# Performance work log

Hardware: AMD Instinct MI355X
Metric: run time of the kernel (lower is better)

The kernel has to match this reference:

```python
import jax, jax.numpy as jnp
import numpy as np

EPS = 1e-5

def _graph_conv(x, src, dst, W, b, N):
    # DGL GraphConv, norm='both': D_out^{-1/2} then aggregate then D_in^{-1/2}
    ones = jnp.ones((src.shape[0],), x.dtype)
    out_deg = jnp.clip(jax.ops.segment_sum(ones, src, num_segments=N), 1.0)
    in_deg = jnp.clip(jax.ops.segment_sum(ones, dst, num_segments=N), 1.0)
    h = (x * (out_deg ** -0.5)[:, None]) @ W          # [N, out] (mult W before gather)
    agg = jax.ops.segment_sum(h[src], dst, num_segments=N)  # [N, out] irregular scatter
    return agg * (in_deg ** -0.5)[:, None] + b

def _bn_relu(h, gamma, beta):
    # BatchNorm1d in training mode: batch stats over node axis (biased var)
    mu = jnp.mean(h, axis=0)
    var = jnp.mean((h - mu) ** 2, axis=0)
    return jax.nn.relu((h - mu) * jax.lax.rsqrt(var + EPS) * gamma + beta)

def setup_inputs() -> dict:
    key = jax.random.key(0)
    ks = jax.random.split(key, 6)
    N, E, F, H, C = 100000, 1000000, 128, 128, 16
    return {
        "x": jax.random.normal(ks[0], (N, F), dtype=jnp.float32),
        "src": jax.random.randint(ks[1], (E,), 0, N, dtype=jnp.int32),
        "dst": jax.random.randint(ks[2], (E,), 0, N, dtype=jnp.int32),
        "W1": jax.random.normal(ks[3], (F, H), dtype=jnp.float32) * 0.05,
        "b1": jnp.zeros((H,), jnp.float32),
        "g1": jnp.ones((H,), jnp.float32),
        "be1": jnp.zeros((H,), jnp.float32),
        "W2": jax.random.normal(ks[4], (H, H), dtype=jnp.float32) * 0.05,
        "b2": jnp.zeros((H,), jnp.float32),
        "g2": jnp.ones((H,), jnp.float32),
        "be2": jnp.zeros((H,), jnp.float32),
        "Wc": jax.random.normal(ks[5], (H, C), dtype=jnp.float32) * 0.05,
        "bc": jnp.zeros((C,), jnp.float32),
    }

def reference(x, src, dst, W1, b1, g1, be1, W2, b2, g2, be2, Wc, bc):
    N = x.shape[0]
    h = _bn_relu(_graph_conv(x, src, dst, W1, b1, N), g1, be1)  # dropout = identity (eval)
    h = _bn_relu(_graph_conv(h, src, dst, W2, b2, N), g2, be2)
    return h @ Wc + bc  # [N, num_cls]
```

## Files before the change

kernel.cpp:

```cpp
#include <hip/hip_runtime.h>

#define FDIM 128
#define MAXDEG 64
#define GATHERB 2048
#define NREP 32

typedef unsigned short ushort_t;
typedef unsigned int uint_t;
typedef __attribute__((ext_vector_type(8))) short short8;
typedef __attribute__((ext_vector_type(16))) float float16;

__device__ __forceinline__ float bflo(uint_t u) { return __uint_as_float(u << 16); }
__device__ __forceinline__ float bfhi(uint_t u) { return __uint_as_float(u & 0xffff0000u); }
__device__ __forceinline__ ushort_t f2bf(float f) {
    uint_t u = __float_as_uint(f);
    return (ushort_t)((u + 0x7fffu + ((u >> 16) & 1u)) >> 16);
}
__device__ __forceinline__ uint_t pack2bf(float lo, float hi) {
    return (uint_t)f2bf(lo) | ((uint_t)f2bf(hi) << 16);
}

__global__ __launch_bounds__(256) void mega1_kernel(
    const float* __restrict__ x, const float* __restrict__ W,
    const int* __restrict__ src, const int* __restrict__ dst,
    int* __restrict__ cs, int* __restrict__ cursor, int* __restrict__ eidx,
    ushort_t* __restrict__ outb, int N, int E,
    int gemmB, int atomicB) {
    int bid = blockIdx.x;
    int t = threadIdx.x;

    int six = atomicB * 6;
    bool isAtomic;
    int idx;
    if (bid < six) {
        int grp = bid / 6, rem = bid % 6;
        if (rem == 5) { isAtomic = true; idx = grp; }
        else { isAtomic = false; idx = grp * 5 + rem; }
    } else {
        isAtomic = false;
        idx = atomicB * 5 + (bid - six);
    }

    if (isAtomic) {
        int stride = atomicB * 256;
        for (int i = idx * 256 + t; i < E; i += stride) {
            int d = dst[i];
            int s = src[i];
            int slot = atomicAdd(&cursor[d], 1);
            if (slot < MAXDEG) eidx[(size_t)d * MAXDEG + slot] = s;
            atomicAdd(&cs[s], 1);
        }
        return;
    }

    if (idx >= gemmB) return;
    __shared__ float xt[16][FDIM];
    int base = idx * 16;
    const float4* x4 = (const float4*)x;
#pragma unroll
    for (int i = 0; i < 2; i++) {
        int ii = t + i * 256;
        int row = ii >> 5, c4 = ii & 31;
        int grow = base + row;
        float4 v = make_float4(0.f, 0.f, 0.f, 0.f);
        if (grow < N) v = x4[(size_t)grow * 32 + c4];
        *(float4*)&xt[row][c4 * 4] = v;
    }
    __syncthreads();
    int rg = t >> 6, c = t & 63;
    float acc[4][2] = {};
    const float* Wc0 = W + c;
    for (int k4 = 0; k4 < 32; k4++) {
        float xv[16];
#pragma unroll
        for (int r = 0; r < 4; r++) {
            float4 tmp = *(const float4*)&xt[rg * 4 + r][k4 * 4];
            xv[r * 4 + 0] = tmp.x; xv[r * 4 + 1] = tmp.y;
            xv[r * 4 + 2] = tmp.z; xv[r * 4 + 3] = tmp.w;
        }
#pragma unroll
        for (int kk = 0; kk < 4; kk++) {
            float w0 = Wc0[(k4 * 4 + kk) * FDIM];
            float w1 = Wc0[(k4 * 4 + kk) * FDIM + 64];
#pragma unroll
            for (int r = 0; r < 4; r++) {
                acc[r][0] = fmaf(xv[r * 4 + kk], w0, acc[r][0]);
                acc[r][1] = fmaf(xv[r * 4 + kk], w1, acc[r][1]);
            }
        }
    }
#pragma unroll
    for (int r = 0; r < 4; r++) {
        int grow = base + rg * 4 + r;
        if (grow < N) {
            outb[(size_t)grow * FDIM + c] = f2bf(acc[r][0]);
            outb[(size_t)grow * FDIM + c + 64] = f2bf(acc[r][1]);
        }
    }
}

template <bool OS>
__global__ __launch_bounds__(256) void gather_kernel(const ushort_t* __restrict__ hb,
                                                     const int* __restrict__ eidx,
                                                     const int* __restrict__ cnt,
                                                     const int* __restrict__ cs,
                                                     const float* __restrict__ b,
                                                     ushort_t* __restrict__ outb,
                                                     float* __restrict__ statsRep, int N) {
    __shared__ float4 redS[256];
    __shared__ float4 redQ[256];
    int t = threadIdx.x;
    int wave = t >> 6, lane = t & 63;
    int half = lane >> 5, sub = lane & 31;
    int gw = blockIdx.x * 4 + wave;
    const uint2* h2 = (const uint2*)hb;
    uint2* o2 = (uint2*)outb;
    float4 bb = ((const float4*)b)[sub];
    float st0 = 0, st1 = 0, st2 = 0, st3 = 0, sq0 = 0, sq1 = 0, sq2 = 0, sq3 = 0;

    for (int node = gw; node < N; node += GATHERB * 4) {
        int deg = cnt[node];
        int e = min(deg, MAXDEG);
        const int* row = eidx + (size_t)node * MAXDEG;
        int ridx = (lane < e) ? row[lane] : 0;
        float scv = 1.f;
        if (OS) scv = (lane < e) ? rsqrtf((float)max(cs[ridx], 1)) : 0.f;

        float a0 = 0, a1 = 0, a2 = 0, a3 = 0;
        float c0 = 0, c1 = 0, c2 = 0, c3 = 0;
        int j = 0;
        for (; j + 3 < e; j += 4) {
            int iA = __shfl(ridx, j + half);
            int iB = __shfl(ridx, j + 2 + half);
            float sA = OS ? __shfl(scv, j + half) : 1.f;
            float sB = OS ? __shfl(scv, j + 2 + half) : 1.f;
            uint2 uA = h2[(size_t)iA * 32 + sub];
            uint2 uB = h2[(size_t)iB * 32 + sub];
            a0 = fmaf(bflo(uA.x), sA, a0); a1 = fmaf(bfhi(uA.x), sA, a1);
            a2 = fmaf(bflo(uA.y), sA, a2); a3 = fmaf(bfhi(uA.y), sA, a3);
            c0 = fmaf(bflo(uB.x), sB, c0); c1 = fmaf(bfhi(uB.x), sB, c1);
            c2 = fmaf(bflo(uB.y), sB, c2); c3 = fmaf(bfhi(uB.y), sB, c3);
        }
        for (; j < e; j += 2) {
            int jj = j + half;
            bool take = jj < e;
            int i0 = __shfl(ridx, take ? jj : (e - 1));
            float s0 = take ? (OS ? __shfl(scv, jj) : 1.f) : 0.f;
            uint2 u = h2[(size_t)i0 * 32 + sub];
            a0 = fmaf(bflo(u.x), s0, a0); a1 = fmaf(bfhi(u.x), s0, a1);
            a2 = fmaf(bflo(u.y), s0, a2); a3 = fmaf(bfhi(u.y), s0, a3);
        }
        a0 += c0; a1 += c1; a2 += c2; a3 += c3;
        a0 += __shfl_xor(a0, 32);
        a1 += __shfl_xor(a1, 32);
        a2 += __shfl_xor(a2, 32);
        a3 += __shfl_xor(a3, 32);
        if (half == 0) {
            float isc = rsqrtf((float)max(deg, 1));
            uint2 o;
            o.x = pack2bf(fmaf(a0, isc, bb.x), fmaf(a1, isc, bb.y));
            o.y = pack2bf(fmaf(a2, isc, bb.z), fmaf(a3, isc, bb.w));
            o2[(size_t)node * 32 + sub] = o;
            float v0 = bflo(o.x), v1 = bfhi(o.x), v2 = bflo(o.y), v3 = bfhi(o.y);
            st0 += v0; st1 += v1; st2 += v2; st3 += v3;
            sq0 = fmaf(v0, v0, sq0); sq1 = fmaf(v1, v1, sq1);
            sq2 = fmaf(v2, v2, sq2); sq3 = fmaf(v3, v3, sq3);
        }
    }

    redS[t] = make_float4(st0, st1, st2, st3);
    redQ[t] = make_float4(sq0, sq1, sq2, sq3);
    __syncthreads();
    if (t < 32) {
        float4 s = make_float4(0, 0, 0, 0), q = make_float4(0, 0, 0, 0);
#pragma unroll
        for (int w = 0; w < 4; w++) {
            float4 a = redS[w * 64 + t];
            float4 z = redQ[w * 64 + t];
            s.x += a.x; s.y += a.y; s.z += a.z; s.w += a.w;
            q.x += z.x; q.y += z.y; q.z += z.z; q.w += z.w;
        }
        float* dstp = statsRep + (size_t)(blockIdx.x & (NREP - 1)) * 256;
        atomicAdd(&dstp[t * 4 + 0], s.x);
        atomicAdd(&dstp[t * 4 + 1], s.y);
        atomicAdd(&dstp[t * 4 + 2], s.z);
        atomicAdd(&dstp[t * 4 + 3], s.w);
        atomicAdd(&dstp[128 + t * 4 + 0], q.x);
        atomicAdd(&dstp[128 + t * 4 + 1], q.y);
        atomicAdd(&dstp[128 + t * 4 + 2], q.z);
        atomicAdd(&dstp[128 + t * 4 + 3], q.w);
    }
}

__global__ __launch_bounds__(256) void gemm2_kernel(const ushort_t* __restrict__ hb,
                                                    const float* __restrict__ W,
                                                    const int* __restrict__ cs,
                                                    const float* __restrict__ statsRep,
                                                    const float* __restrict__ g,
                                                    const float* __restrict__ be,
                                                    ushort_t* __restrict__ outb, int N,
                                                    float invN) {
    __shared__ ushort_t zt[64][136];
    __shared__ ushort_t wt[128][136];
    __shared__ float Ash[FDIM], Bsh[FDIM];
    int t = threadIdx.x;
    int base = blockIdx.x * 64;

    if (t < FDIM) {
        float s = 0.f, q = 0.f;
        for (int r = 0; r < NREP; r++) {
            s += statsRep[r * 256 + t];
            q += statsRep[r * 256 + 128 + t];
        }
        float mu = s * invN;
        float var = q * invN - mu * mu;
        float a = g[t] * rsqrtf(var + 1e-5f);
        Ash[t] = a;
        Bsh[t] = be[t] - mu * a;
    }
    for (int i = t; i < FDIM * FDIM; i += 256) {
        int k = i >> 7, n = i & 127;
        wt[n][k] = f2bf(W[i]);
    }
    __syncthreads();

    const uint_t* h1 = (const uint_t*)hb;
    for (int i = t; i < 64 * 64; i += 256) {
        int row = i >> 6, cp = i & 63;
        int grow = base + row;
        uint_t o = 0;
        if (grow < N) {
            uint_t u = h1[(size_t)grow * 64 + cp];
            float s = rsqrtf((float)max(cs[grow], 1));
            float v0 = fmaxf(fmaf(bflo(u), Ash[cp * 2], Bsh[cp * 2]), 0.f) * s;
            float v1 = fmaxf(fmaf(bfhi(u), Ash[cp * 2 + 1], Bsh[cp * 2 + 1]), 0.f) * s;
            o = pack2bf(v0, v1);
        }
        *(uint_t*)&zt[row][cp * 2] = o;
    }
    __syncthreads();

    int wv = t >> 6, lane = t & 63;
    int rt = wv >> 1;
    int m = lane & 31;
    int kg = lane >> 5;

    short8 af[8];
#pragma unroll
    for (int kk = 0; kk < 8; kk++)
        af[kk] = *(const short8*)&zt[rt * 32 + m][kk * 16 + kg * 8];

#pragma unroll
    for (int cc = 0; cc < 2; cc++) {
        int ct = (wv & 1) * 2 + cc;
        float16 acc = {0, 0, 0, 0, 0, 0, 0, 0, 0, 0, 0, 0, 0, 0, 0, 0};
#pragma unroll
        for (int kk = 0; kk < 8; kk++) {
            short8 bf = *(const short8*)&wt[ct * 32 + m][kk * 16 + kg * 8];
            acc = __builtin_amdgcn_mfma_f32_32x32x16_bf16(af[kk], bf, acc, 0, 0, 0);
        }
        int col = ct * 32 + m;
#pragma unroll
        for (int r = 0; r < 16; r++) {
            int row = base + rt * 32 + (r & 3) + 8 * (r >> 2) + 4 * kg;
            if (row < N) outb[(size_t)row * FDIM + col] = f2bf(acc[r]);
        }
    }
}

__global__ __launch_bounds__(256) void cls_kernel(const ushort_t* __restrict__ hb,
                                                  const float* __restrict__ Wc,
                                                  const float* __restrict__ bc,
                                                  const float* __restrict__ statsRep,
                                                  const float* __restrict__ g,
                                                  const float* __restrict__ be,
                                                  float* __restrict__ out, int N, float invN) {
    __shared__ float wcl[FDIM * 16];
    __shared__ float red[16][256];
    __shared__ float Ash[FDIM], Bsh[FDIM];
    int t = threadIdx.x;
    int base = blockIdx.x * 64;
#pragma unroll
    for (int i = 0; i < 8; i++) wcl[t + i * 256] = Wc[t + i * 256];
    if (t < FDIM) {
        float s = 0.f, q = 0.f;
        for (int r = 0; r < NREP; r++) {
            s += statsRep[r * 256 + t];
            q += statsRep[r * 256 + 128 + t];
        }
        float mu = s * invN;
        float var = q * invN - mu * mu;
        float a = g[t] * rsqrtf(var + 1e-5f);
        Ash[t] = a;
        Bsh[t] = be[t] - mu * a;
    }
    __syncthreads();

    int node = base + (t >> 2);
    int q4 = t & 3;
    float acc[16];
#pragma unroll
    for (int c = 0; c < 16; c++) acc[c] = 0.f;

    if (node < N) {
        const uint2* hu2 = (const uint2*)((const uint_t*)hb + (size_t)node * 64 + q4 * 16);
        const float* Af = Ash + q4 * 32;
        const float* Bf = Bsh + q4 * 32;
#pragma unroll 1
        for (int kk = 0; kk < 8; kk++) {
            uint2 u = hu2[kk];
            float4 ab = *(const float4*)&Af[kk * 4];
            float4 bb = *(const float4*)&Bf[kk * 4];
            float v0 = fmaxf(fmaf(bflo(u.x), ab.x, bb.x), 0.f);
            float v1 = fmaxf(fmaf(bfhi(u.x), ab.y, bb.y), 0.f);
            float v2 = fmaxf(fmaf(bflo(u.y), ab.z, bb.z), 0.f);
            float v3 = fmaxf(fmaf(bfhi(u.y), ab.w, bb.w), 0.f);
            int k0 = q4 * 32 + kk * 4;
            const float* w0 = &wcl[k0 * 16];
#pragma unroll
            for (int c = 0; c < 16; c++) {
                float s = fmaf(v0, w0[c], fmaf(v1, w0[16 + c], fmaf(v2, w0[32 + c], v3 * w0[48 + c])));
                acc[c] += s;
            }
        }
    }
#pragma unroll
    for (int c = 0; c < 16; c++) red[c][t] = acc[c];
    __syncthreads();
#pragma unroll
    for (int i = t; i < 64 * 16; i += 256) {
        int n = i >> 4, c = i & 15;
        float4 p = *(const float4*)&red[c][n * 4];
        int grow = base + n;
        if (grow < N) out[(size_t)grow * 16 + c] = (p.x + p.y) + (p.z + p.w) + bc[c];
    }
}

extern "C" void kernel_launch(void* const* d_in, const int* in_sizes, int n_in,
                              void* d_out, int out_size, void* d_ws, size_t ws_size,
                              hipStream_t stream) {
    const float* x  = (const float*)d_in[0];
    const int* src  = (const int*)d_in[1];
    const int* dst  = (const int*)d_in[2];
    const float* W1 = (const float*)d_in[3];
    const float* b1 = (const float*)d_in[4];
    const float* g1 = (const float*)d_in[5];
    const float* be1= (const float*)d_in[6];
    const float* W2 = (const float*)d_in[7];
    const float* b2 = (const float*)d_in[8];
    const float* g2 = (const float*)d_in[9];
    const float* be2= (const float*)d_in[10];
    const float* Wc = (const float*)d_in[11];
    const float* bc = (const float*)d_in[12];
    float* out = (float*)d_out;

    int N = in_sizes[0] / FDIM;
    int E = in_sizes[1];
    size_t NB = (size_t)N * FDIM;

    ushort_t* bufA = (ushort_t*)d_ws;
    ushort_t* bufB = bufA + NB;
    int* cs        = (int*)(bufB + NB);
    int* cursor    = cs + N;
    float* statsR1 = (float*)(cursor + N);
    float* statsR2 = statsR1 + NREP * 256;
    int* eidx      = (int*)(statsR2 + NREP * 256);

    hipMemsetAsync(cs, 0, ((size_t)2 * N + 2 * NREP * 256) * sizeof(int), stream);

    int gemmB = (N + 15) / 16;
    int atomicB = (gemmB + 4) / 5;
    int totalB = gemmB + atomicB;

    mega1_kernel<<<totalB, 256, 0, stream>>>(
        x, W1, src, dst, cs, cursor, eidx, bufA, N, E, gemmB, atomicB);

    float invN = 1.0f / N;

    gather_kernel<true><<<GATHERB, 256, 0, stream>>>(bufA, eidx, cursor, cs, b1, bufB, statsR1, N);

    gemm2_kernel<<<(N + 63) / 64, 256, 0, stream>>>(bufB, W2, cs, statsR1, g1, be1, bufA, N, invN);
    gather_kernel<false><<<GATHERB, 256, 0, stream>>>(bufA, eidx, cursor, nullptr, b2, bufB, statsR2, N);

    cls_kernel<<<(N + 63) / 64, 256, 0, stream>>>(bufB, Wc, bc, statsR2, g2, be2, out, N, invN);
}
```

Measured before the change: 380.7 us.

## Assign one node per half-wave in gather kernel instead of one per wave

The gather kernel now processes two nodes per wave, one per 32-lane half, instead of splitting one node's edges across both halves. This removes the cross-half shuffle reduction and lets every half-wave write and accumulate statistics, and the block reduction is adjusted to sum 8 groups of 32 lanes. Each half now walks its node's neighbour list serially with 4-way unrolling. Degree imbalance between the two nodes sharing a wave can cause divergence, and nodes with more than 32 edges fall back to a slower scalar loop.

```diff
diff --git a/kernel.cpp b/kernel.cpp
--- a/kernel.cpp
+++ b/kernel.cpp
@@ -112,28 +112,61 @@
     int t = threadIdx.x;
     int wave = t >> 6, lane = t & 63;
     int half = lane >> 5, sub = lane & 31;
-    int gw = blockIdx.x * 4 + wave;
+    int hofs = half * 32;
     const uint2* h2 = (const uint2*)hb;
     uint2* o2 = (uint2*)outb;
     float4 bb = ((const float4*)b)[sub];
     float st0 = 0, st1 = 0, st2 = 0, st3 = 0, sq0 = 0, sq1 = 0, sq2 = 0, sq3 = 0;
 
-    for (int node = gw; node < N; node += GATHERB * 4) {
-        int deg = cnt[node];
+    int pairCount = (N + 1) >> 1;
+    for (int p = blockIdx.x * 4 + wave; p < pairCount; p += GATHERB * 4) {
+        int node = 2 * p + half;
+        bool valid = node < N;
+        int deg = valid ? cnt[node] : 0;
         int e = min(deg, MAXDEG);
-        const int* row = eidx + (size_t)node * MAXDEG;
-        int ridx = (lane < e) ? row[lane] : 0;
-        float scv = 1.f;
-        if (OS) scv = (lane < e) ? rsqrtf((float)max(cs[ridx], 1)) : 0.f;
+        int e1 = min(e, 32);
+
+        const int* rowSelf = eidx + (size_t)node * MAXDEG;
+        int ridx = (valid && sub < e) ? rowSelf[sub] : 0;
+        float scv = 0.f;
+        if (OS) scv = (valid && sub < e) ? rsqrtf((float)max(cs[ridx], 1)) : 0.f;
+        int ridx2 = 0;
+        float scv2 = 0.f;
+        if (e > 32) {
+            ridx2 = (sub + 32 < e) ? rowSelf[32 + sub] : 0;
+            if (OS) scv2 = (sub + 32 < e) ? rsqrtf((float)max(cs[ridx2], 1)) : 0.f;
+        }
 
         float a0 = 0, a1 = 0, a2 = 0, a3 = 0;
         float c0 = 0, c1 = 0, c2 = 0, c3 = 0;
         int j = 0;
-        for (; j + 3 < e; j += 4) {
-            int iA = __shfl(ridx, j + half);
-            int iB = __shfl(ridx, j + 2 + half);
-            float sA = OS ? __shfl(scv, j + half) : 1.f;
-            float sB = OS ? __shfl(scv, j + 2 + half) : 1.f;
+        for (; j + 3 < e1; j += 4) {
+            int iA = __shfl(ridx, hofs + j);
+            int iB = __shfl(ridx, hofs + j + 1);
+            int iC = __shfl(ridx, hofs + j + 2);
+            int iD = __shfl(ridx, hofs + j + 3);
+            float sA = OS ? __shfl(scv, hofs + j) : 1.f;
+            float sB = OS ? __shfl(scv, hofs + j + 1) : 1.f;
+            float sC = OS ? __shfl(scv, hofs + j + 2) : 1.f;
+            float sD = OS ? __shfl(scv, hofs + j + 3) : 1.f;
+            uint2 uA = h2[(size_t)iA * 32 + sub];
+            uint2 uB = h2[(size_t)iB * 32 + sub];
+            uint2 uC = h2[(size_t)iC * 32 + sub];
+            uint2 uD = h2[(size_t)iD * 32 + sub];
+            a0 = fmaf(bflo(uA.x), sA, a0); a1 = fmaf(bfhi(uA.x), sA, a1);
+            a2 = fmaf(bflo(uA.y), sA, a2); a3 = fmaf(bfhi(uA.y), sA, a3);
+            c0 = fmaf(bflo(uB.x), sB, c0); c1 = fmaf(bfhi(uB.x), sB, c1);
+            c2 = fmaf(bflo(uB.y), sB, c2); c3 = fmaf(bfhi(uB.y), sB, c3);
+            a0 = fmaf(bflo(uC.x), sC, a0); a1 = fmaf(bfhi(uC.x), sC, a1);
+            a2 = fmaf(bflo(uC.y), sC, a2); a3 = fmaf(bfhi(uC.y), sC, a3);
+            c0 = fmaf(bflo(uD.x), sD, c0); c1 = fmaf(bfhi(uD.x), sD, c1);
+            c2 = fmaf(bflo(uD.y), sD, c2); c3 = fmaf(bfhi(uD.y), sD, c3);
+        }
+        for (; j + 1 < e1; j += 2) {
+            int iA = __shfl(ridx, hofs + j);
+            int iB = __shfl(ridx, hofs + j + 1);
+            float sA = OS ? __shfl(scv, hofs + j) : 1.f;
+            float sB = OS ? __shfl(scv, hofs + j + 1) : 1.f;
             uint2 uA = h2[(size_t)iA * 32 + sub];
             uint2 uB = h2[(size_t)iB * 32 + sub];
             a0 = fmaf(bflo(uA.x), sA, a0); a1 = fmaf(bfhi(uA.x), sA, a1);
@@ -141,21 +174,24 @@
             c0 = fmaf(bflo(uB.x), sB, c0); c1 = fmaf(bfhi(uB.x), sB, c1);
             c2 = fmaf(bflo(uB.y), sB, c2); c3 = fmaf(bfhi(uB.y), sB, c3);
         }
-        for (; j < e; j += 2) {
-            int jj = j + half;
-            bool take = jj < e;
-            int i0 = __shfl(ridx, take ? jj : (e - 1));
-            float s0 = take ? (OS ? __shfl(scv, jj) : 1.f) : 0.f;
-            uint2 u = h2[(size_t)i0 * 32 + sub];
-            a0 = fmaf(bflo(u.x), s0, a0); a1 = fmaf(bfhi(u.x), s0, a1);
-            a2 = fmaf(bflo(u.y), s0, a2); a3 = fmaf(bfhi(u.y), s0, a3);
+        if (j < e1) {
+            int iA = __shfl(ridx, hofs + j);
+            float sA = OS ? __shfl(scv, hofs + j) : 1.f;
+            uint2 uA = h2[(size_t)iA * 32 + sub];
+            a0 = fmaf(bflo(uA.x), sA, a0); a1 = fmaf(bfhi(uA.x), sA, a1);
+            a2 = fmaf(bflo(uA.y), sA, a2); a3 = fmaf(bfhi(uA.y), sA, a3);
+            j++;
+        }
+        for (j = 32; j < e; j++) {
+            int iA = __shfl(ridx2, hofs + (j - 32));
+            float sA = OS ? __shfl(scv2, hofs + (j - 32)) : 1.f;
+            uint2 uA = h2[(size_t)iA * 32 + sub];
+            a0 = fmaf(bflo(uA.x), sA, a0); a1 = fmaf(bfhi(uA.x), sA, a1);
+            a2 = fmaf(bflo(uA.y), sA, a2); a3 = fmaf(bfhi(uA.y), sA, a3);
         }
         a0 += c0; a1 += c1; a2 += c2; a3 += c3;
-        a0 += __shfl_xor(a0, 32);
-        a1 += __shfl_xor(a1, 32);
-        a2 += __shfl_xor(a2, 32);
-        a3 += __shfl_xor(a3, 32);
-        if (half == 0) {
+
+        if (valid) {
             float isc = rsqrtf((float)max(deg, 1));
             uint2 o;
             o.x = pack2bf(fmaf(a0, isc, bb.x), fmaf(a1, isc, bb.y));
@@ -174,9 +210,9 @@
     if (t < 32) {
         float4 s = make_float4(0, 0, 0, 0), q = make_float4(0, 0, 0, 0);
 #pragma unroll
-        for (int w = 0; w < 4; w++) {
-            float4 a = redS[w * 64 + t];
-            float4 z = redQ[w * 64 + t];
+        for (int w = 0; w < 8; w++) {
+            float4 a = redS[w * 32 + t];
+            float4 z = redQ[w * 32 + t];
             s.x += a.x; s.y += a.y; s.z += a.z; s.w += a.w;
             q.x += z.x; q.y += z.y; q.z += z.z; q.w += z.w;
         }
```

After: 384.5 us. About the same (+1.0%).
